# Kernel optimization log

Measured on AMD Instinct MI355X. Metric: run time of the kernel, lower is better.

Reference implementation:

```python
import jax, jax.numpy as jnp
import numpy as np

NEG_SLOPE = 0.2  # PyG GATConv default leaky_relu slope
EPS = 1e-16     # PyG softmax denominator epsilon


def gat_conv(x, src, dst, W, att_src, att_dst, bias, concat, num_nodes):
    """PyG-style GATConv (eval mode, dropout disabled).
    x: [N, F_in]; W: [F_in, H*C]; att_src/att_dst: [H, C]; bias: [H*C] or [C].
    Messages flow src -> dst; softmax is per destination node."""
    H, C = att_src.shape
    h = (x @ W).reshape(num_nodes, H, C)                      # [N,H,C]
    a_src = jnp.sum(h * att_src[None], axis=-1)               # [N,H]
    a_dst = jnp.sum(h * att_dst[None], axis=-1)               # [N,H]
    e = jax.nn.leaky_relu(a_src[src] + a_dst[dst], NEG_SLOPE) # [E,H]
    # numerically-stable segment softmax over edges grouped by dst
    m = jax.ops.segment_max(e, dst, num_segments=num_nodes)   # [N,H]
    ex = jnp.exp(e - m[dst])                                  # [E,H]
    s = jax.ops.segment_sum(ex, dst, num_segments=num_nodes)  # [N,H]
    alpha = ex / (s[dst] + EPS)                               # [E,H]
    msg = h[src] * alpha[..., None]                           # [E,H,C]
    out = jax.ops.segment_sum(msg, dst, num_segments=num_nodes)  # [N,H,C]
    if concat:
        out = out.reshape(num_nodes, H * C)
    else:
        out = out.mean(axis=1)                                # [N,C]
    return out + bias, alpha


def setup_inputs() -> dict:
    key = jax.random.key(0)
    ks = jax.random.split(key, 20)
    N, E = 50000, 500000
    F_node = 128       # num_node_features
    SED = 128          # sentence_embedding_dim
    HID = 64           # hidden_channels
    H = 2              # num_heads

    def g(k, shape, scale=0.05):
        return jax.random.normal(k, shape, dtype=jnp.float32) * scale

    return {
        "x": jax.random.normal(ks[0], (N, SED), dtype=jnp.float32),
        "edge_index": jax.random.randint(ks[1], (2, E), 0, N, dtype=jnp.int64),
        "cls_emb": jax.random.normal(ks[2], (768,), dtype=jnp.float32),
        # fc0: Linear(768, SED)
        "fc0_w": g(ks[3], (SED, 768)), "fc0_b": g(ks[4], (SED,)),
        # conv1: GATConv(2*SED -> HID, heads=H, concat=True)
        "W1": g(ks[5], (2 * SED, H * HID)),
        "att_src1": g(ks[6], (H, HID)), "att_dst1": g(ks[7], (H, HID)),
        "bias1": g(ks[8], (H * HID,)),
        # conv2: GATConv(H*HID -> F_node, heads=H, concat=False)
        "W2": g(ks[9], (H * HID, H * F_node)),
        "att_src2": g(ks[10], (H, F_node)), "att_dst2": g(ks[11], (H, F_node)),
        "bias2": g(ks[12], (F_node,)),
        # edge MLP head
        "fc2_w": g(ks[13], (F_node, 2 * F_node)), "fc2_b": g(ks[14], (F_node,)),
        "fc3_w": g(ks[15], (1, F_node)), "fc3_b": g(ks[16], (1,)),
    }


def reference(x, edge_index, cls_emb, fc0_w, fc0_b,
              W1, att_src1, att_dst1, bias1,
              W2, att_src2, att_dst2, bias2,
              fc2_w, fc2_b, fc3_w, fc3_b):
    N = x.shape[0]
    src, dst = edge_index[0], edge_index[1]
    # sentence embedding projection + broadcast-concat to every node
    sent = fc0_w @ cls_emb + fc0_b                                # [SED]
    h = jnp.concatenate([x, jnp.broadcast_to(sent, (N, sent.shape[0]))], axis=1)
    h, _ = gat_conv(h, src, dst, W1, att_src1, att_dst1, bias1, True, N)
    h = jax.nn.elu(h)
    h, _ = gat_conv(h, src, dst, W2, att_src2, att_dst2, bias2, False, N)
    # edge head: gather endpoints, concat, MLP, sigmoid
    edge_input = jnp.concatenate([h[src], h[dst]], axis=1)        # [E, 2*F]
    z = jax.nn.relu(edge_input @ fc2_w.T + fc2_b)                 # [E, F]
    logits = z @ fc3_w.T + fc3_b                                  # [E, 1]
    return jax.nn.sigmoid(logits)
```

## Files before the change

### kernel.cpp

```cpp
#include <hip/hip_runtime.h>
#include <hip/hip_bf16.h>
#include <math.h>


typedef short short8 __attribute__((ext_vector_type(8)));
typedef float floatx4 __attribute__((ext_vector_type(4)));
typedef float v2f __attribute__((ext_vector_type(2)));
typedef unsigned uint2v __attribute__((ext_vector_type(2)));

__device__ __forceinline__ v2f bfpair(unsigned v) {
    uint2v t; t.x = v << 16; t.y = v & 0xFFFF0000u;
    return __builtin_bit_cast(v2f, t);
}
__device__ __forceinline__ unsigned short bfbits(float f) {
    return __builtin_bit_cast(unsigned short, __float2bfloat16(f));
}
__device__ __forceinline__ unsigned packbf(float a, float b) {
    return ((unsigned)bfbits(b) << 16) | (unsigned)bfbits(a);
}
__device__ __forceinline__ float lrelu(float v) { return v > 0.f ? v : 0.2f * v; }

__global__ void prep_kernel(const float* __restrict__ cls, const float* __restrict__ fc0_w,
                            const float* __restrict__ fc0_b, const float* __restrict__ W1,
                            const float* __restrict__ W2, const float* __restrict__ fc2_w,
                            float* __restrict__ c1,
                            __hip_bfloat16* __restrict__ w1frag,
                            __hip_bfloat16* __restrict__ w2frag,
                            __hip_bfloat16* __restrict__ fc2frag) {
    int tid = threadIdx.x;
    if (blockIdx.x == 0) {
        __shared__ float s_sent[128];
        if (tid < 128) {
            float acc = fc0_b[tid];
            const float* row = fc0_w + (size_t)tid * 768;
            for (int k = 0; k < 768; ++k) acc += row[k] * cls[k];
            s_sent[tid] = acc;
        }
        __syncthreads();
        if (tid < 128) {
            float acc = 0.f;
            for (int k = 0; k < 128; ++k) acc += s_sent[k] * W1[(128 + k) * 128 + tid];
            c1[tid] = acc;
        }
    }
    int gstride = gridDim.x * blockDim.x;
    int g = blockIdx.x * blockDim.x + tid;
    for (int i = g; i < 16384; i += gstride) {
        int j = i & 7, l = (i >> 3) & 63, nt = (i >> 9) & 7, kt = (i >> 12) & 3;
        int k = kt * 32 + (l >> 4) * 8 + j;
        int n = nt * 16 + (l & 15);
        w1frag[i] = __float2bfloat16(W1[k * 128 + n]);
    }
    for (int i = g; i < 32768; i += gstride) {
        int j = i & 7, l = (i >> 3) & 63, nt = (i >> 9) & 15, kt = (i >> 13) & 3;
        int k = kt * 32 + (l >> 4) * 8 + j;
        int n = nt * 16 + (l & 15);
        w2frag[i] = __float2bfloat16(W2[k * 256 + n]);
    }
    for (int i = g; i < 32768; i += gstride) {
        int j = i & 7, l = (i >> 3) & 63, nt = (i >> 9) & 15, kt = (i >> 13) & 3;
        int k = kt * 32 + (l >> 4) * 8 + j;
        int n = nt * 16 + (l & 15);
        float v = (n < 128) ? fc2_w[n * 256 + k] : fc2_w[(n - 128) * 256 + 128 + k];
        fc2frag[i] = __float2bfloat16(v);
    }
}

__global__ void __launch_bounds__(256) bsum_kernel(const int* __restrict__ counts,
                                                   int* __restrict__ bsum, int N) {
    int base = blockIdx.x * 1024;
    int tid = threadIdx.x;
    int v = 0;
    #pragma unroll
    for (int k = 0; k < 4; ++k) {
        int idx = base + k * 256 + tid;
        if (idx < N) v += counts[idx];
    }
    #pragma unroll
    for (int off = 1; off < 64; off <<= 1) v += __shfl_xor(v, off, 64);
    __shared__ int ws[4];
    if ((tid & 63) == 0) ws[tid >> 6] = v;
    __syncthreads();
    if (tid == 0) bsum[blockIdx.x] = ws[0] + ws[1] + ws[2] + ws[3];
}

__global__ void top_scan_kernel(const int* __restrict__ bsum, int* __restrict__ boff, int nb) {
    int lane = threadIdx.x;
    int v = (lane < nb) ? bsum[lane] : 0;
    int x = v;
    #pragma unroll
    for (int off = 1; off < 64; off <<= 1) {
        int t = __shfl_up(x, off, 64);
        if (lane >= off) x += t;
    }
    if (lane < nb) boff[lane] = x - v;
}

__global__ void __launch_bounds__(1024) local_scan_kernel(const int* __restrict__ counts,
                                                          const int* __restrict__ boff,
                                                          int* __restrict__ row, int* __restrict__ woff,
                                                          int N, int E) {
    int tid = threadIdx.x, lane = tid & 63, wv = tid >> 6;
    int base = blockIdx.x * 1024;
    __shared__ int wsum[16];
    int v = (base + tid < N) ? counts[base + tid] : 0;
    int x = v;
    #pragma unroll
    for (int off = 1; off < 64; off <<= 1) {
        int t = __shfl_up(x, off, 64);
        if (lane >= off) x += t;
    }
    if (lane == 63) wsum[wv] = x;
    __syncthreads();
    if (wv == 0 && lane < 16) {
        int y = wsum[lane];
        #pragma unroll
        for (int off = 1; off < 16; off <<= 1) {
            int t = __shfl_up(y, off, 64);
            if (lane >= off) y += t;
        }
        wsum[lane] = y;
    }
    __syncthreads();
    int excl = boff[blockIdx.x] + (wv ? wsum[wv - 1] : 0) + x - v;
    if (base + tid < N) { row[base + tid] = excl; woff[base + tid] = excl; }
    if (blockIdx.x == 0 && tid == 0) row[N] = E;
}

__global__ void scatter_kernel(const int* __restrict__ src, const int* __restrict__ dst,
                               int* __restrict__ woff, int* __restrict__ srcs, int E) {
    int e = blockIdx.x * blockDim.x + threadIdx.x;
    if (e < E) {
        int pos = atomicAdd(&woff[dst[e]], 1);
        srcs[pos] = src[e];
    }
}

__global__ void __launch_bounds__(256) gemm1_count_kernel(
        const float* __restrict__ x, const __hip_bfloat16* __restrict__ wfrag,
        const float* __restrict__ c1, const float* __restrict__ att_s, const float* __restrict__ att_d,
        __hip_bfloat16* __restrict__ h1bf, float* __restrict__ a_src, float* __restrict__ a_dst,
        const int* __restrict__ dst, int* __restrict__ counts, int E, int G1, int N) {
    if ((int)blockIdx.x >= G1) {
        int e = ((int)blockIdx.x - G1) * 256 + threadIdx.x;
        if (e < E) atomicAdd(&counts[dst[e]], 1);
        return;
    }
    int lane = threadIdx.x & 63, wv = threadIdx.x >> 6;
    int lo = lane & 15, quad = lane >> 4;
    int rowbase = ((int)blockIdx.x * 4 + wv) * 16;
    if (rowbase >= N) return;
    int arow = rowbase + lo; if (arow >= N) arow = N - 1;
    const float* ap = x + (size_t)arow * 128 + quad * 8;
    floatx4 acc[8];
    #pragma unroll
    for (int nt = 0; nt < 8; ++nt) acc[nt] = (floatx4){0.f, 0.f, 0.f, 0.f};
    const short8* bf = (const short8*)wfrag;
    #pragma unroll
    for (int kt = 0; kt < 4; ++kt) {
        float4 fa = *(const float4*)(ap + kt * 32);
        float4 fb = *(const float4*)(ap + kt * 32 + 4);
        short8 a;
        a[0] = (short)bfbits(fa.x); a[1] = (short)bfbits(fa.y);
        a[2] = (short)bfbits(fa.z); a[3] = (short)bfbits(fa.w);
        a[4] = (short)bfbits(fb.x); a[5] = (short)bfbits(fb.y);
        a[6] = (short)bfbits(fb.z); a[7] = (short)bfbits(fb.w);
        #pragma unroll
        for (int nt = 0; nt < 8; ++nt)
            acc[nt] = __builtin_amdgcn_mfma_f32_16x16x32_bf16(a, bf[(kt * 8 + nt) * 64 + lane], acc[nt], 0, 0, 0);
    }
    float ps0[4] = {0,0,0,0}, ps1[4] = {0,0,0,0}, pd0[4] = {0,0,0,0}, pd1[4] = {0,0,0,0};
    #pragma unroll
    for (int nt = 0; nt < 8; ++nt) {
        int ch = nt * 16 + lo;
        float cv = c1[ch], as_v = att_s[ch], ad_v = att_d[ch];
        #pragma unroll
        for (int r = 0; r < 4; ++r) {
            int row = rowbase + quad * 4 + r;
            float val = acc[nt][r] + cv;
            if (row < N) ((unsigned short*)h1bf)[(size_t)row * 128 + ch] = bfbits(val);
            if (nt < 4) { ps0[r] += val * as_v; pd0[r] += val * ad_v; }
            else        { ps1[r] += val * as_v; pd1[r] += val * ad_v; }
        }
    }
    #pragma unroll
    for (int r = 0; r < 4; ++r) {
        int row = rowbase + quad * 4 + r;
        float v0 = ps0[r], v1 = ps1[r], v2 = pd0[r], v3 = pd1[r];
        #pragma unroll
        for (int off = 1; off < 16; off <<= 1) {
            v0 += __shfl_xor(v0, off, 64); v1 += __shfl_xor(v1, off, 64);
            v2 += __shfl_xor(v2, off, 64); v3 += __shfl_xor(v3, off, 64);
        }
        if (lo == 0 && row < N) {
            a_src[row * 2 + 0] = v0; a_src[row * 2 + 1] = v1;
            a_dst[row * 2 + 0] = v2; a_dst[row * 2 + 1] = v3;
        }
    }
}

__global__ void __launch_bounds__(256) agg1_csr_kernel(
        const int* __restrict__ row, const int* __restrict__ srcs,
        const float* __restrict__ a_src, const float* __restrict__ a_dst,
        const unsigned* __restrict__ h1u, const float* __restrict__ bias1,
        unsigned* __restrict__ hmid_u, int N) {
    int tid = threadIdx.x;
    int d = blockIdx.x * 16 + (tid >> 4);
    if (d >= N) return;
    int q = tid & 15;
    int beg = row[d], end = row[d + 1];
    float2 adp = ((const float2*)a_dst)[d];
    float den0 = 0.f, den1 = 0.f;
    v2f facc2[4];
    #pragma unroll
    for (int m = 0; m < 4; ++m) facc2[m] = (v2f){0.f, 0.f};
    for (int i = beg; i < end; i += 2) {
        int s0 = srcs[i];
        bool has1 = (i + 1) < end;
        int s1 = has1 ? srcs[i + 1] : s0;
        float2 as0 = ((const float2*)a_src)[s0];
        float2 as1 = ((const float2*)a_src)[s1];
        uint4 u0 = ((const uint4*)(h1u + (size_t)s0 * 64))[q];
        uint4 u1 = ((const uint4*)(h1u + (size_t)s1 * 64))[q];
        float e00 = __expf(lrelu(as0.x + adp.x));
        float e01 = __expf(lrelu(as0.y + adp.y));
        float e10 = has1 ? __expf(lrelu(as1.x + adp.x)) : 0.f;
        float e11 = has1 ? __expf(lrelu(as1.y + adp.y)) : 0.f;
        den0 += e00 + e10;
        den1 += e01 + e11;
        float w0 = (q < 8) ? e00 : e01;
        float w1 = (q < 8) ? e10 : e11;
        facc2[0] += bfpair(u0.x) * w0 + bfpair(u1.x) * w1;
        facc2[1] += bfpair(u0.y) * w0 + bfpair(u1.y) * w1;
        facc2[2] += bfpair(u0.z) * w0 + bfpair(u1.z) * w1;
        facc2[3] += bfpair(u0.w) * w0 + bfpair(u1.w) * w1;
    }
    float inv = 1.f / (((q < 8) ? den0 : den1) + 1e-16f);
    int c0 = 8 * q;
    float v[8];
    #pragma unroll
    for (int m = 0; m < 4; ++m) {
        float va = facc2[m].x * inv + bias1[c0 + 2 * m];
        float vb = facc2[m].y * inv + bias1[c0 + 2 * m + 1];
        v[2 * m]     = va > 0.f ? va : expm1f(va);
        v[2 * m + 1] = vb > 0.f ? vb : expm1f(vb);
    }
    uint4 o;
    o.x = packbf(v[0], v[1]); o.y = packbf(v[2], v[3]);
    o.z = packbf(v[4], v[5]); o.w = packbf(v[6], v[7]);
    ((uint4*)(hmid_u + (size_t)d * 64))[q] = o;
}

__global__ void __launch_bounds__(256) gemm2_mfma_kernel(
        const __hip_bfloat16* __restrict__ hmid, const __hip_bfloat16* __restrict__ wfrag,
        const float* __restrict__ att_s, const float* __restrict__ att_d,
        __hip_bfloat16* __restrict__ h2pre, float* __restrict__ a_src, float* __restrict__ a_dst, int N) {
    int lane = threadIdx.x & 63, wv = threadIdx.x >> 6;
    int lo = lane & 15, quad = lane >> 4;
    int rowbase = (blockIdx.x * 4 + wv) * 16;
    if (rowbase >= N) return;
    int arow = rowbase + lo; if (arow >= N) arow = N - 1;
    const __hip_bfloat16* ap = hmid + (size_t)arow * 128 + quad * 8;
    floatx4 acc[16];
    #pragma unroll
    for (int nt = 0; nt < 16; ++nt) acc[nt] = (floatx4){0.f, 0.f, 0.f, 0.f};
    const short8* bf = (const short8*)wfrag;
    #pragma unroll
    for (int kt = 0; kt < 4; ++kt) {
        short8 a = *(const short8*)(ap + kt * 32);
        #pragma unroll
        for (int nt = 0; nt < 16; ++nt)
            acc[nt] = __builtin_amdgcn_mfma_f32_16x16x32_bf16(a, bf[(kt * 16 + nt) * 64 + lane], acc[nt], 0, 0, 0);
    }
    float ps0[4] = {0,0,0,0}, ps1[4] = {0,0,0,0}, pd0[4] = {0,0,0,0}, pd1[4] = {0,0,0,0};
    #pragma unroll
    for (int nt = 0; nt < 16; ++nt) {
        int ch = nt * 16 + lo;
        float as_v = att_s[ch], ad_v = att_d[ch];
        #pragma unroll
        for (int r = 0; r < 4; ++r) {
            int row = rowbase + quad * 4 + r;
            float val = acc[nt][r];
            if (row < N) ((unsigned short*)h2pre)[(size_t)row * 256 + ch] = bfbits(val);
            if (nt < 8) { ps0[r] += val * as_v; pd0[r] += val * ad_v; }
            else        { ps1[r] += val * as_v; pd1[r] += val * ad_v; }
        }
    }
    #pragma unroll
    for (int r = 0; r < 4; ++r) {
        int row = rowbase + quad * 4 + r;
        float v0 = ps0[r], v1 = ps1[r], v2 = pd0[r], v3 = pd1[r];
        #pragma unroll
        for (int off = 1; off < 16; off <<= 1) {
            v0 += __shfl_xor(v0, off, 64); v1 += __shfl_xor(v1, off, 64);
            v2 += __shfl_xor(v2, off, 64); v3 += __shfl_xor(v3, off, 64);
        }
        if (lo == 0 && row < N) {
            a_src[row * 2 + 0] = v0; a_src[row * 2 + 1] = v1;
            a_dst[row * 2 + 0] = v2; a_dst[row * 2 + 1] = v3;
        }
    }
}

__global__ void __launch_bounds__(256) agg2_csr_kernel(
        const int* __restrict__ row, const int* __restrict__ srcs,
        const float* __restrict__ a_src, const float* __restrict__ a_dst,
        const unsigned* __restrict__ h2u, const float* __restrict__ bias2,
        unsigned* __restrict__ h2bf_u, int N) {
    int tid = threadIdx.x;
    int d = blockIdx.x * 8 + (tid >> 5);
    if (d >= N) return;
    int q = tid & 31;
    int beg = row[d], end = row[d + 1];
    float2 adp = ((const float2*)a_dst)[d];
    float den0 = 0.f, den1 = 0.f;
    v2f facc2[4];
    #pragma unroll
    for (int m = 0; m < 4; ++m) facc2[m] = (v2f){0.f, 0.f};
    for (int i = beg; i < end; i += 2) {
        int s0 = srcs[i];
        bool has1 = (i + 1) < end;
        int s1 = has1 ? srcs[i + 1] : s0;
        float2 as0 = ((const float2*)a_src)[s0];
        float2 as1 = ((const float2*)a_src)[s1];
        uint4 u0 = ((const uint4*)(h2u + (size_t)s0 * 128))[q];
        uint4 u1 = ((const uint4*)(h2u + (size_t)s1 * 128))[q];
        float e00 = __expf(lrelu(as0.x + adp.x));
        float e01 = __expf(lrelu(as0.y + adp.y));
        float e10 = has1 ? __expf(lrelu(as1.x + adp.x)) : 0.f;
        float e11 = has1 ? __expf(lrelu(as1.y + adp.y)) : 0.f;
        den0 += e00 + e10;
        den1 += e01 + e11;
        float w0 = (q < 16) ? e00 : e01;
        float w1 = (q < 16) ? e10 : e11;
        facc2[0] += bfpair(u0.x) * w0 + bfpair(u1.x) * w1;
        facc2[1] += bfpair(u0.y) * w0 + bfpair(u1.y) * w1;
        facc2[2] += bfpair(u0.z) * w0 + bfpair(u1.z) * w1;
        facc2[3] += bfpair(u0.w) * w0 + bfpair(u1.w) * w1;
    }
    float inv = 0.5f / (((q < 16) ? den0 : den1) + 1e-16f);
    #pragma unroll
    for (int m = 0; m < 4; ++m) {
        facc2[m] *= inv;
        facc2[m].x += __shfl_xor(facc2[m].x, 16, 64);
        facc2[m].y += __shfl_xor(facc2[m].y, 16, 64);
    }
    if (q < 16) {
        int c0 = 8 * q;
        uint4 o;
        o.x = packbf(facc2[0].x + bias2[c0 + 0], facc2[0].y + bias2[c0 + 1]);
        o.y = packbf(facc2[1].x + bias2[c0 + 2], facc2[1].y + bias2[c0 + 3]);
        o.z = packbf(facc2[2].x + bias2[c0 + 4], facc2[2].y + bias2[c0 + 5]);
        o.w = packbf(facc2[3].x + bias2[c0 + 6], facc2[3].y + bias2[c0 + 7]);
        ((uint4*)(h2bf_u + (size_t)d * 64))[q] = o;
    }
}

__global__ void __launch_bounds__(256) zsd_mfma_kernel(
        const __hip_bfloat16* __restrict__ h2bf, const __hip_bfloat16* __restrict__ wfrag,
        const float* __restrict__ fc2_b, __hip_bfloat16* __restrict__ zsd, int N) {
    int lane = threadIdx.x & 63, wv = threadIdx.x >> 6;
    int lo = lane & 15, quad = lane >> 4;
    int rowbase = (blockIdx.x * 4 + wv) * 16;
    if (rowbase >= N) return;
    int arow = rowbase + lo; if (arow >= N) arow = N - 1;
    const __hip_bfloat16* ap = h2bf + (size_t)arow * 128 + quad * 8;
    floatx4 acc[16];
    #pragma unroll
    for (int nt = 0; nt < 16; ++nt) acc[nt] = (floatx4){0.f, 0.f, 0.f, 0.f};
    const short8* bf = (const short8*)wfrag;
    #pragma unroll
    for (int kt = 0; kt < 4; ++kt) {
        short8 a = *(const short8*)(ap + kt * 32);
        #pragma unroll
        for (int nt = 0; nt < 16; ++nt)
            acc[nt] = __builtin_amdgcn_mfma_f32_16x16x32_bf16(a, bf[(kt * 16 + nt) * 64 + lane], acc[nt], 0, 0, 0);
    }
    #pragma unroll
    for (int nt = 0; nt < 16; ++nt) {
        int ch = nt * 16 + lo;
        float bv = (nt >= 8) ? fc2_b[ch - 128] : 0.f;
        #pragma unroll
        for (int r = 0; r < 4; ++r) {
            int row = rowbase + quad * 4 + r;
            if (row < N) ((unsigned short*)zsd)[(size_t)row * 256 + ch] = bfbits(acc[nt][r] + bv);
        }
    }
}

__global__ void __launch_bounds__(256) edge_zsd_kernel(
        const int* __restrict__ src, const int* __restrict__ dst,
        const unsigned* __restrict__ zsd_u, const float* __restrict__ fc3_w,
        const float* __restrict__ fc3_b, float* __restrict__ out, int E) {
    int lane = threadIdx.x & 63, wv = threadIdx.x >> 6;
    int g = lane >> 5, r = (lane >> 4) & 1, q = lane & 15;
    int base = (blockIdx.x * 4 + wv) * 16;
    if (base >= E) return;
    v2f f30 = {fc3_w[8 * q + 4 * r + 0], fc3_w[8 * q + 4 * r + 1]};
    v2f f31 = {fc3_w[8 * q + 4 * r + 2], fc3_w[8 * q + 4 * r + 3]};
    float b3 = fc3_b[0];
    int nodes[8];
    #pragma unroll
    for (int j = 0; j < 8; ++j) {
        int e = base + 2 * j + g;
        int ec = e < E ? e : E - 1;
        nodes[j] = r ? dst[ec] : src[ec];
    }
    uint4 rows[8];
    #pragma unroll
    for (int j = 0; j < 8; ++j)
        rows[j] = ((const uint4*)(zsd_u + (size_t)nodes[j] * 128 + (r << 6)))[q];
    #pragma unroll
    for (int j = 0; j < 8; ++j) {
        uint4 mine = rows[j];
        unsigned sx = (unsigned)__shfl_xor((int)mine.x, 16, 64);
        unsigned sy = (unsigned)__shfl_xor((int)mine.y, 16, 64);
        unsigned sz = (unsigned)__shfl_xor((int)mine.z, 16, 64);
        unsigned sw = (unsigned)__shfl_xor((int)mine.w, 16, 64);
        unsigned mA = r ? mine.z : mine.x;
        unsigned mB = r ? mine.w : mine.y;
        unsigned oA = r ? sz : sx;
        unsigned oB = r ? sw : sy;
        v2f sA = bfpair(mA) + bfpair(oA);
        v2f sB = bfpair(mB) + bfpair(oB);
        sA.x = fmaxf(sA.x, 0.f); sA.y = fmaxf(sA.y, 0.f);
        sB.x = fmaxf(sB.x, 0.f); sB.y = fmaxf(sB.y, 0.f);
        v2f p2 = sA * f30 + sB * f31;
        float p = p2.x + p2.y;
        #pragma unroll
        for (int off = 1; off < 32; off <<= 1) p += __shfl_xor(p, off, 64);
        int e = base + 2 * j + g;
        if ((lane & 31) == 0 && e < E)
            out[e] = 1.f / (1.f + expf(-(p + b3)));
    }
}

extern "C" void kernel_launch(void* const* d_in, const int* in_sizes, int n_in,
                              void* d_out, int out_size, void* d_ws, size_t ws_size,
                              hipStream_t stream) {
    const float* x      = (const float*)d_in[0];
    const int*   ei     = (const int*)d_in[1];
    const float* cls    = (const float*)d_in[2];
    const float* fc0_w  = (const float*)d_in[3];
    const float* fc0_b  = (const float*)d_in[4];
    const float* W1     = (const float*)d_in[5];
    const float* att_s1 = (const float*)d_in[6];
    const float* att_d1 = (const float*)d_in[7];
    const float* bias1  = (const float*)d_in[8];
    const float* W2     = (const float*)d_in[9];
    const float* att_s2 = (const float*)d_in[10];
    const float* att_d2 = (const float*)d_in[11];
    const float* bias2  = (const float*)d_in[12];
    const float* fc2_w  = (const float*)d_in[13];
    const float* fc2_b  = (const float*)d_in[14];
    const float* fc3_w  = (const float*)d_in[15];
    const float* fc3_b  = (const float*)d_in[16];
    float* out = (float*)d_out;

    int N = in_sizes[0] / 128;
    int E = in_sizes[1] / 2;
    const int* src = ei;
    const int* dst = ei + E;
    int nb = (N + 1023) / 1024;

    float* w = (float*)d_ws;
    size_t off = 0;
    auto alloc = [&](size_t n) { float* p = w + off; off += (n + 63) & ~(size_t)63; return p; };
    float* c1      = alloc(128);
    float* w1fragf = alloc(16384 / 2);
    float* w2fragf = alloc(32768 / 2);
    float* fc2fragf= alloc(32768 / 2);
    float* a_s1    = alloc((size_t)N * 2);
    float* a_d1    = alloc((size_t)N * 2);
    float* a_s2    = alloc((size_t)N * 2);
    float* a_d2    = alloc((size_t)N * 2);
    float* h1bff   = alloc((size_t)N * 64);
    float* hmidf   = alloc((size_t)N * 64);
    float* h2pref  = alloc((size_t)N * 128);
    float* h2bff   = alloc((size_t)N * 64);
    float* zsdf    = alloc((size_t)N * 128);
    int* counts = (int*)alloc(N);
    int* rowp   = (int*)alloc(N + 1);
    int* woff   = (int*)alloc(N);
    int* srcs   = (int*)alloc(E);
    int* bsum   = (int*)alloc(64);
    int* boff   = (int*)alloc(64);
    __hip_bfloat16* w1frag = (__hip_bfloat16*)w1fragf;
    __hip_bfloat16* w2frag = (__hip_bfloat16*)w2fragf;
    __hip_bfloat16* fc2frag= (__hip_bfloat16*)fc2fragf;
    __hip_bfloat16* hmid   = (__hip_bfloat16*)hmidf;
    __hip_bfloat16* h2pre  = (__hip_bfloat16*)h2pref;
    __hip_bfloat16* h2bf   = (__hip_bfloat16*)h2bff;
    __hip_bfloat16* h1bf   = (__hip_bfloat16*)h1bff;
    __hip_bfloat16* zsd    = (__hip_bfloat16*)zsdf;

    hipMemsetAsync(counts, 0, sizeof(int) * (size_t)N, stream);

    prep_kernel<<<64, 256, 0, stream>>>(cls, fc0_w, fc0_b, W1, W2, fc2_w, c1, w1frag, w2frag, fc2frag);
    int G1 = (N + 63) / 64;
    int G2 = (E + 255) / 256;
    gemm1_count_kernel<<<G1 + G2, 256, 0, stream>>>(x, w1frag, c1, att_s1, att_d1, h1bf, a_s1, a_d1,
                                                    dst, counts, E, G1, N);
    bsum_kernel<<<nb, 256, 0, stream>>>(counts, bsum, N);
    top_scan_kernel<<<1, 64, 0, stream>>>(bsum, boff, nb);
    local_scan_kernel<<<nb, 1024, 0, stream>>>(counts, boff, rowp, woff, N, E);
    scatter_kernel<<<(E + 255) / 256, 256, 0, stream>>>(src, dst, woff, srcs, E);
    agg1_csr_kernel<<<(N + 15) / 16, 256, 0, stream>>>(rowp, srcs, a_s1, a_d1, (const unsigned*)h1bf, bias1, (unsigned*)hmid, N);
    gemm2_mfma_kernel<<<(N + 63) / 64, 256, 0, stream>>>(hmid, w2frag, att_s2, att_d2, h2pre, a_s2, a_d2, N);
    agg2_csr_kernel<<<(N + 7) / 8, 256, 0, stream>>>(rowp, srcs, a_s2, a_d2, (const unsigned*)h2pre, bias2, (unsigned*)h2bf, N);
    zsd_mfma_kernel<<<(N + 63) / 64, 256, 0, stream>>>(h2bf, fc2frag, fc2_b, zsd, N);
    edge_zsd_kernel<<<(E + 63) / 64, 256, 0, stream>>>(src, dst, (const unsigned*)zsd, fc3_w, fc3_b, out, E);
}
```

Baseline: 336.3 us.

## Fuse all stages into one cooperative persistent kernel with grid syncs

Replaces the sequence of about eleven kernel launches and a memset with a single cooperative mega-kernel that loops over tiles persistently and uses grid.sync between stages. The aim is to remove per-launch overhead and the gaps between dependent kernels. In exchange, every stage shares one register and occupancy budget capped by the heaviest stage (launch_bounds 256,4). It also adds grid-wide barrier costs and host occupancy queries on each call, and the local scan is restructured to four elements per thread.

```diff
diff --git a/kernel.cpp b/kernel.cpp
--- a/kernel.cpp
+++ b/kernel.cpp
@@ -1,6 +1,9 @@
 #include <hip/hip_runtime.h>
+#include <hip/hip_cooperative_groups.h>
 #include <hip/hip_bf16.h>
 #include <math.h>
+
+namespace cg = cooperative_groups;
 
 
 typedef short short8 __attribute__((ext_vector_type(8)));
@@ -20,448 +23,441 @@
 }
 __device__ __forceinline__ float lrelu(float v) { return v > 0.f ? v : 0.2f * v; }
 
-__global__ void prep_kernel(const float* __restrict__ cls, const float* __restrict__ fc0_w,
-                            const float* __restrict__ fc0_b, const float* __restrict__ W1,
-                            const float* __restrict__ W2, const float* __restrict__ fc2_w,
-                            float* __restrict__ c1,
-                            __hip_bfloat16* __restrict__ w1frag,
-                            __hip_bfloat16* __restrict__ w2frag,
-                            __hip_bfloat16* __restrict__ fc2frag) {
-    int tid = threadIdx.x;
+struct MegaParams {
+    const float* x; const int* src; const int* dst;
+    const float* cls; const float* fc0_w; const float* fc0_b;
+    const float* W1; const float* att_s1; const float* att_d1; const float* bias1;
+    const float* W2; const float* att_s2; const float* att_d2; const float* bias2;
+    const float* fc2_w; const float* fc2_b; const float* fc3_w; const float* fc3_b;
+    float* out;
+    float* c1; __hip_bfloat16* w1frag; __hip_bfloat16* w2frag; __hip_bfloat16* fc2frag;
+    float* a_s1; float* a_d1; float* a_s2; float* a_d2;
+    __hip_bfloat16* h1bf; __hip_bfloat16* hmid; __hip_bfloat16* h2pre;
+    __hip_bfloat16* h2bf; __hip_bfloat16* zsd;
+    int* counts; int* rowp; int* woff; int* srcs; int* bsum; int* boff;
+    int N, E, nb;
+};
+
+__global__ void __launch_bounds__(256, 4) mega_kernel(MegaParams p) {
+    cg::grid_group grid = cg::this_grid();
+    const int tid = threadIdx.x;
+    const int G = gridDim.x;
+    const int lane = tid & 63, wv = tid >> 6;
+    const int lo = lane & 15, quad = lane >> 4;
+    const int N = p.N, E = p.E;
+
+    __shared__ float s_sent[128];
+    __shared__ int s_wsum[16];
+
+    for (int i = blockIdx.x * 256 + tid; i < N; i += G * 256) p.counts[i] = 0;
     if (blockIdx.x == 0) {
-        __shared__ float s_sent[128];
         if (tid < 128) {
-            float acc = fc0_b[tid];
-            const float* row = fc0_w + (size_t)tid * 768;
-            for (int k = 0; k < 768; ++k) acc += row[k] * cls[k];
+            float acc = p.fc0_b[tid];
+            const float* row = p.fc0_w + (size_t)tid * 768;
+            for (int k = 0; k < 768; ++k) acc += row[k] * p.cls[k];
             s_sent[tid] = acc;
         }
         __syncthreads();
         if (tid < 128) {
             float acc = 0.f;
-            for (int k = 0; k < 128; ++k) acc += s_sent[k] * W1[(128 + k) * 128 + tid];
-            c1[tid] = acc;
-        }
-    }
-    int gstride = gridDim.x * blockDim.x;
-    int g = blockIdx.x * blockDim.x + tid;
-    for (int i = g; i < 16384; i += gstride) {
-        int j = i & 7, l = (i >> 3) & 63, nt = (i >> 9) & 7, kt = (i >> 12) & 3;
-        int k = kt * 32 + (l >> 4) * 8 + j;
-        int n = nt * 16 + (l & 15);
-        w1frag[i] = __float2bfloat16(W1[k * 128 + n]);
-    }
-    for (int i = g; i < 32768; i += gstride) {
-        int j = i & 7, l = (i >> 3) & 63, nt = (i >> 9) & 15, kt = (i >> 13) & 3;
-        int k = kt * 32 + (l >> 4) * 8 + j;
-        int n = nt * 16 + (l & 15);
-        w2frag[i] = __float2bfloat16(W2[k * 256 + n]);
-    }
-    for (int i = g; i < 32768; i += gstride) {
-        int j = i & 7, l = (i >> 3) & 63, nt = (i >> 9) & 15, kt = (i >> 13) & 3;
-        int k = kt * 32 + (l >> 4) * 8 + j;
-        int n = nt * 16 + (l & 15);
-        float v = (n < 128) ? fc2_w[n * 256 + k] : fc2_w[(n - 128) * 256 + 128 + k];
-        fc2frag[i] = __float2bfloat16(v);
-    }
-}
-
-__global__ void __launch_bounds__(256) bsum_kernel(const int* __restrict__ counts,
-                                                   int* __restrict__ bsum, int N) {
-    int base = blockIdx.x * 1024;
-    int tid = threadIdx.x;
-    int v = 0;
-    #pragma unroll
-    for (int k = 0; k < 4; ++k) {
-        int idx = base + k * 256 + tid;
-        if (idx < N) v += counts[idx];
-    }
-    #pragma unroll
-    for (int off = 1; off < 64; off <<= 1) v += __shfl_xor(v, off, 64);
-    __shared__ int ws[4];
-    if ((tid & 63) == 0) ws[tid >> 6] = v;
-    __syncthreads();
-    if (tid == 0) bsum[blockIdx.x] = ws[0] + ws[1] + ws[2] + ws[3];
-}
-
-__global__ void top_scan_kernel(const int* __restrict__ bsum, int* __restrict__ boff, int nb) {
-    int lane = threadIdx.x;
-    int v = (lane < nb) ? bsum[lane] : 0;
-    int x = v;
-    #pragma unroll
-    for (int off = 1; off < 64; off <<= 1) {
-        int t = __shfl_up(x, off, 64);
-        if (lane >= off) x += t;
-    }
-    if (lane < nb) boff[lane] = x - v;
-}
-
-__global__ void __launch_bounds__(1024) local_scan_kernel(const int* __restrict__ counts,
-                                                          const int* __restrict__ boff,
-                                                          int* __restrict__ row, int* __restrict__ woff,
-                                                          int N, int E) {
-    int tid = threadIdx.x, lane = tid & 63, wv = tid >> 6;
-    int base = blockIdx.x * 1024;
-    __shared__ int wsum[16];
-    int v = (base + tid < N) ? counts[base + tid] : 0;
-    int x = v;
-    #pragma unroll
-    for (int off = 1; off < 64; off <<= 1) {
-        int t = __shfl_up(x, off, 64);
-        if (lane >= off) x += t;
-    }
-    if (lane == 63) wsum[wv] = x;
-    __syncthreads();
-    if (wv == 0 && lane < 16) {
-        int y = wsum[lane];
+            for (int k = 0; k < 128; ++k) acc += s_sent[k] * p.W1[(128 + k) * 128 + tid];
+            p.c1[tid] = acc;
+        }
+    }
+    {
+        int g = blockIdx.x * 256 + tid, gs = G * 256;
+        for (int i = g; i < 16384; i += gs) {
+            int j = i & 7, l = (i >> 3) & 63, nt = (i >> 9) & 7, kt = (i >> 12) & 3;
+            int k = kt * 32 + (l >> 4) * 8 + j;
+            int n = nt * 16 + (l & 15);
+            p.w1frag[i] = __float2bfloat16(p.W1[k * 128 + n]);
+        }
+        for (int i = g; i < 32768; i += gs) {
+            int j = i & 7, l = (i >> 3) & 63, nt = (i >> 9) & 15, kt = (i >> 13) & 3;
+            int k = kt * 32 + (l >> 4) * 8 + j;
+            int n = nt * 16 + (l & 15);
+            p.w2frag[i] = __float2bfloat16(p.W2[k * 256 + n]);
+        }
+        for (int i = g; i < 32768; i += gs) {
+            int j = i & 7, l = (i >> 3) & 63, nt = (i >> 9) & 15, kt = (i >> 13) & 3;
+            int k = kt * 32 + (l >> 4) * 8 + j;
+            int n = nt * 16 + (l & 15);
+            float v = (n < 128) ? p.fc2_w[n * 256 + k] : p.fc2_w[(n - 128) * 256 + 128 + k];
+            p.fc2frag[i] = __float2bfloat16(v);
+        }
+    }
+    grid.sync();
+
+    {
+        int T = (N + 63) / 64;
+        const short8* bf = (const short8*)p.w1frag;
+        for (int tb = blockIdx.x; tb < T; tb += G) {
+            int rowbase = (tb * 4 + wv) * 16;
+            if (rowbase < N) {
+                int arow = rowbase + lo; if (arow >= N) arow = N - 1;
+                const float* ap = p.x + (size_t)arow * 128 + quad * 8;
+                floatx4 acc[8];
+                #pragma unroll
+                for (int nt = 0; nt < 8; ++nt) acc[nt] = (floatx4){0.f, 0.f, 0.f, 0.f};
+                #pragma unroll
+                for (int kt = 0; kt < 4; ++kt) {
+                    float4 fa = *(const float4*)(ap + kt * 32);
+                    float4 fb = *(const float4*)(ap + kt * 32 + 4);
+                    short8 a;
+                    a[0] = (short)bfbits(fa.x); a[1] = (short)bfbits(fa.y);
+                    a[2] = (short)bfbits(fa.z); a[3] = (short)bfbits(fa.w);
+                    a[4] = (short)bfbits(fb.x); a[5] = (short)bfbits(fb.y);
+                    a[6] = (short)bfbits(fb.z); a[7] = (short)bfbits(fb.w);
+                    #pragma unroll
+                    for (int nt = 0; nt < 8; ++nt)
+                        acc[nt] = __builtin_amdgcn_mfma_f32_16x16x32_bf16(a, bf[(kt * 8 + nt) * 64 + lane], acc[nt], 0, 0, 0);
+                }
+                float ps0[4] = {0,0,0,0}, ps1[4] = {0,0,0,0}, pd0[4] = {0,0,0,0}, pd1[4] = {0,0,0,0};
+                #pragma unroll
+                for (int nt = 0; nt < 8; ++nt) {
+                    int ch = nt * 16 + lo;
+                    float cv = p.c1[ch], as_v = p.att_s1[ch], ad_v = p.att_d1[ch];
+                    #pragma unroll
+                    for (int r = 0; r < 4; ++r) {
+                        int row = rowbase + quad * 4 + r;
+                        float val = acc[nt][r] + cv;
+                        if (row < N) ((unsigned short*)p.h1bf)[(size_t)row * 128 + ch] = bfbits(val);
+                        if (nt < 4) { ps0[r] += val * as_v; pd0[r] += val * ad_v; }
+                        else        { ps1[r] += val * as_v; pd1[r] += val * ad_v; }
+                    }
+                }
+                #pragma unroll
+                for (int r = 0; r < 4; ++r) {
+                    int row = rowbase + quad * 4 + r;
+                    float v0 = ps0[r], v1 = ps1[r], v2 = pd0[r], v3 = pd1[r];
+                    #pragma unroll
+                    for (int off = 1; off < 16; off <<= 1) {
+                        v0 += __shfl_xor(v0, off, 64); v1 += __shfl_xor(v1, off, 64);
+                        v2 += __shfl_xor(v2, off, 64); v3 += __shfl_xor(v3, off, 64);
+                    }
+                    if (lo == 0 && row < N) {
+                        p.a_s1[row * 2 + 0] = v0; p.a_s1[row * 2 + 1] = v1;
+                        p.a_d1[row * 2 + 0] = v2; p.a_d1[row * 2 + 1] = v3;
+                    }
+                }
+            }
+        }
+        for (int e = blockIdx.x * 256 + tid; e < E; e += G * 256)
+            atomicAdd(&p.counts[p.dst[e]], 1);
+    }
+    grid.sync();
+
+    for (int tb = blockIdx.x; tb < p.nb; tb += G) {
+        int base = tb * 1024;
+        int v = 0;
         #pragma unroll
-        for (int off = 1; off < 16; off <<= 1) {
-            int t = __shfl_up(y, off, 64);
-            if (lane >= off) y += t;
-        }
-        wsum[lane] = y;
-    }
-    __syncthreads();
-    int excl = boff[blockIdx.x] + (wv ? wsum[wv - 1] : 0) + x - v;
-    if (base + tid < N) { row[base + tid] = excl; woff[base + tid] = excl; }
-    if (blockIdx.x == 0 && tid == 0) row[N] = E;
-}
-
-__global__ void scatter_kernel(const int* __restrict__ src, const int* __restrict__ dst,
-                               int* __restrict__ woff, int* __restrict__ srcs, int E) {
-    int e = blockIdx.x * blockDim.x + threadIdx.x;
-    if (e < E) {
-        int pos = atomicAdd(&woff[dst[e]], 1);
-        srcs[pos] = src[e];
-    }
-}
-
-__global__ void __launch_bounds__(256) gemm1_count_kernel(
-        const float* __restrict__ x, const __hip_bfloat16* __restrict__ wfrag,
-        const float* __restrict__ c1, const float* __restrict__ att_s, const float* __restrict__ att_d,
-        __hip_bfloat16* __restrict__ h1bf, float* __restrict__ a_src, float* __restrict__ a_dst,
-        const int* __restrict__ dst, int* __restrict__ counts, int E, int G1, int N) {
-    if ((int)blockIdx.x >= G1) {
-        int e = ((int)blockIdx.x - G1) * 256 + threadIdx.x;
-        if (e < E) atomicAdd(&counts[dst[e]], 1);
-        return;
-    }
-    int lane = threadIdx.x & 63, wv = threadIdx.x >> 6;
-    int lo = lane & 15, quad = lane >> 4;
-    int rowbase = ((int)blockIdx.x * 4 + wv) * 16;
-    if (rowbase >= N) return;
-    int arow = rowbase + lo; if (arow >= N) arow = N - 1;
-    const float* ap = x + (size_t)arow * 128 + quad * 8;
-    floatx4 acc[8];
-    #pragma unroll
-    for (int nt = 0; nt < 8; ++nt) acc[nt] = (floatx4){0.f, 0.f, 0.f, 0.f};
-    const short8* bf = (const short8*)wfrag;
-    #pragma unroll
-    for (int kt = 0; kt < 4; ++kt) {
-        float4 fa = *(const float4*)(ap + kt * 32);
-        float4 fb = *(const float4*)(ap + kt * 32 + 4);
-        short8 a;
-        a[0] = (short)bfbits(fa.x); a[1] = (short)bfbits(fa.y);
-        a[2] = (short)bfbits(fa.z); a[3] = (short)bfbits(fa.w);
-        a[4] = (short)bfbits(fb.x); a[5] = (short)bfbits(fb.y);
-        a[6] = (short)bfbits(fb.z); a[7] = (short)bfbits(fb.w);
+        for (int k = 0; k < 4; ++k) {
+            int idx = base + k * 256 + tid;
+            if (idx < N) v += p.counts[idx];
+        }
         #pragma unroll
-        for (int nt = 0; nt < 8; ++nt)
-            acc[nt] = __builtin_amdgcn_mfma_f32_16x16x32_bf16(a, bf[(kt * 8 + nt) * 64 + lane], acc[nt], 0, 0, 0);
-    }
-    float ps0[4] = {0,0,0,0}, ps1[4] = {0,0,0,0}, pd0[4] = {0,0,0,0}, pd1[4] = {0,0,0,0};
-    #pragma unroll
-    for (int nt = 0; nt < 8; ++nt) {
-        int ch = nt * 16 + lo;
-        float cv = c1[ch], as_v = att_s[ch], ad_v = att_d[ch];
+        for (int off = 1; off < 64; off <<= 1) v += __shfl_xor(v, off, 64);
+        if (lane == 0) s_wsum[wv] = v;
+        __syncthreads();
+        if (tid == 0) p.bsum[tb] = s_wsum[0] + s_wsum[1] + s_wsum[2] + s_wsum[3];
+        __syncthreads();
+    }
+    grid.sync();
+
+    if (blockIdx.x == 0 && tid < 64) {
+        int v = (tid < p.nb) ? p.bsum[tid] : 0;
+        int x = v;
         #pragma unroll
-        for (int r = 0; r < 4; ++r) {
-            int row = rowbase + quad * 4 + r;
-            float val = acc[nt][r] + cv;
-            if (row < N) ((unsigned short*)h1bf)[(size_t)row * 128 + ch] = bfbits(val);
-            if (nt < 4) { ps0[r] += val * as_v; pd0[r] += val * ad_v; }
-            else        { ps1[r] += val * as_v; pd1[r] += val * ad_v; }
-        }
-    }
-    #pragma unroll
-    for (int r = 0; r < 4; ++r) {
-        int row = rowbase + quad * 4 + r;
-        float v0 = ps0[r], v1 = ps1[r], v2 = pd0[r], v3 = pd1[r];
+        for (int off = 1; off < 64; off <<= 1) {
+            int t = __shfl_up(x, off, 64);
+            if (tid >= off) x += t;
+        }
+        if (tid < p.nb) p.boff[tid] = x - v;
+    }
+    grid.sync();
+
+    for (int tb = blockIdx.x; tb < p.nb; tb += G) {
+        int i0 = tb * 1024 + tid * 4;
+        int c[4]; int tsum = 0;
         #pragma unroll
-        for (int off = 1; off < 16; off <<= 1) {
-            v0 += __shfl_xor(v0, off, 64); v1 += __shfl_xor(v1, off, 64);
-            v2 += __shfl_xor(v2, off, 64); v3 += __shfl_xor(v3, off, 64);
-        }
-        if (lo == 0 && row < N) {
-            a_src[row * 2 + 0] = v0; a_src[row * 2 + 1] = v1;
-            a_dst[row * 2 + 0] = v2; a_dst[row * 2 + 1] = v3;
-        }
-    }
-}
-
-__global__ void __launch_bounds__(256) agg1_csr_kernel(
-        const int* __restrict__ row, const int* __restrict__ srcs,
-        const float* __restrict__ a_src, const float* __restrict__ a_dst,
-        const unsigned* __restrict__ h1u, const float* __restrict__ bias1,
-        unsigned* __restrict__ hmid_u, int N) {
-    int tid = threadIdx.x;
-    int d = blockIdx.x * 16 + (tid >> 4);
-    if (d >= N) return;
-    int q = tid & 15;
-    int beg = row[d], end = row[d + 1];
-    float2 adp = ((const float2*)a_dst)[d];
-    float den0 = 0.f, den1 = 0.f;
-    v2f facc2[4];
-    #pragma unroll
-    for (int m = 0; m < 4; ++m) facc2[m] = (v2f){0.f, 0.f};
-    for (int i = beg; i < end; i += 2) {
-        int s0 = srcs[i];
-        bool has1 = (i + 1) < end;
-        int s1 = has1 ? srcs[i + 1] : s0;
-        float2 as0 = ((const float2*)a_src)[s0];
-        float2 as1 = ((const float2*)a_src)[s1];
-        uint4 u0 = ((const uint4*)(h1u + (size_t)s0 * 64))[q];
-        uint4 u1 = ((const uint4*)(h1u + (size_t)s1 * 64))[q];
-        float e00 = __expf(lrelu(as0.x + adp.x));
-        float e01 = __expf(lrelu(as0.y + adp.y));
-        float e10 = has1 ? __expf(lrelu(as1.x + adp.x)) : 0.f;
-        float e11 = has1 ? __expf(lrelu(as1.y + adp.y)) : 0.f;
-        den0 += e00 + e10;
-        den1 += e01 + e11;
-        float w0 = (q < 8) ? e00 : e01;
-        float w1 = (q < 8) ? e10 : e11;
-        facc2[0] += bfpair(u0.x) * w0 + bfpair(u1.x) * w1;
-        facc2[1] += bfpair(u0.y) * w0 + bfpair(u1.y) * w1;
-        facc2[2] += bfpair(u0.z) * w0 + bfpair(u1.z) * w1;
-        facc2[3] += bfpair(u0.w) * w0 + bfpair(u1.w) * w1;
-    }
-    float inv = 1.f / (((q < 8) ? den0 : den1) + 1e-16f);
-    int c0 = 8 * q;
-    float v[8];
-    #pragma unroll
-    for (int m = 0; m < 4; ++m) {
-        float va = facc2[m].x * inv + bias1[c0 + 2 * m];
-        float vb = facc2[m].y * inv + bias1[c0 + 2 * m + 1];
-        v[2 * m]     = va > 0.f ? va : expm1f(va);
-        v[2 * m + 1] = vb > 0.f ? vb : expm1f(vb);
-    }
-    uint4 o;
-    o.x = packbf(v[0], v[1]); o.y = packbf(v[2], v[3]);
-    o.z = packbf(v[4], v[5]); o.w = packbf(v[6], v[7]);
-    ((uint4*)(hmid_u + (size_t)d * 64))[q] = o;
-}
-
-__global__ void __launch_bounds__(256) gemm2_mfma_kernel(
-        const __hip_bfloat16* __restrict__ hmid, const __hip_bfloat16* __restrict__ wfrag,
-        const float* __restrict__ att_s, const float* __restrict__ att_d,
-        __hip_bfloat16* __restrict__ h2pre, float* __restrict__ a_src, float* __restrict__ a_dst, int N) {
-    int lane = threadIdx.x & 63, wv = threadIdx.x >> 6;
-    int lo = lane & 15, quad = lane >> 4;
-    int rowbase = (blockIdx.x * 4 + wv) * 16;
-    if (rowbase >= N) return;
-    int arow = rowbase + lo; if (arow >= N) arow = N - 1;
-    const __hip_bfloat16* ap = hmid + (size_t)arow * 128 + quad * 8;
-    floatx4 acc[16];
-    #pragma unroll
-    for (int nt = 0; nt < 16; ++nt) acc[nt] = (floatx4){0.f, 0.f, 0.f, 0.f};
-    const short8* bf = (const short8*)wfrag;
-    #pragma unroll
-    for (int kt = 0; kt < 4; ++kt) {
-        short8 a = *(const short8*)(ap + kt * 32);
+        for (int k = 0; k < 4; ++k) {
+            c[k] = (i0 + k < N) ? p.counts[i0 + k] : 0;
+            tsum += c[k];
+        }
+        int x = tsum;
         #pragma unroll
-        for (int nt = 0; nt < 16; ++nt)
-            acc[nt] = __builtin_amdgcn_mfma_f32_16x16x32_bf16(a, bf[(kt * 16 + nt) * 64 + lane], acc[nt], 0, 0, 0);
-    }
-    float ps0[4] = {0,0,0,0}, ps1[4] = {0,0,0,0}, pd0[4] = {0,0,0,0}, pd1[4] = {0,0,0,0};
-    #pragma unroll
-    for (int nt = 0; nt < 16; ++nt) {
-        int ch = nt * 16 + lo;
-        float as_v = att_s[ch], ad_v = att_d[ch];
+        for (int off = 1; off < 64; off <<= 1) {
+            int t = __shfl_up(x, off, 64);
+            if (lane >= off) x += t;
+        }
+        if (lane == 63) s_wsum[wv] = x;
+        __syncthreads();
+        int add = 0;
+        for (int w = 0; w < wv; ++w) add += s_wsum[w];
+        int run = p.boff[tb] + add + x - tsum;
         #pragma unroll
-        for (int r = 0; r < 4; ++r) {
-            int row = rowbase + quad * 4 + r;
-            float val = acc[nt][r];
-            if (row < N) ((unsigned short*)h2pre)[(size_t)row * 256 + ch] = bfbits(val);
-            if (nt < 8) { ps0[r] += val * as_v; pd0[r] += val * ad_v; }
-            else        { ps1[r] += val * as_v; pd1[r] += val * ad_v; }
-        }
-    }
-    #pragma unroll
-    for (int r = 0; r < 4; ++r) {
-        int row = rowbase + quad * 4 + r;
-        float v0 = ps0[r], v1 = ps1[r], v2 = pd0[r], v3 = pd1[r];
-        #pragma unroll
-        for (int off = 1; off < 16; off <<= 1) {
-            v0 += __shfl_xor(v0, off, 64); v1 += __shfl_xor(v1, off, 64);
-            v2 += __shfl_xor(v2, off, 64); v3 += __shfl_xor(v3, off, 64);
-        }
-        if (lo == 0 && row < N) {
-            a_src[row * 2 + 0] = v0; a_src[row * 2 + 1] = v1;
-            a_dst[row * 2 + 0] = v2; a_dst[row * 2 + 1] = v3;
-        }
-    }
-}
-
-__global__ void __launch_bounds__(256) agg2_csr_kernel(
-        const int* __restrict__ row, const int* __restrict__ srcs,
-        const float* __restrict__ a_src, const float* __restrict__ a_dst,
-        const unsigned* __restrict__ h2u, const float* __restrict__ bias2,
-        unsigned* __restrict__ h2bf_u, int N) {
-    int tid = threadIdx.x;
-    int d = blockIdx.x * 8 + (tid >> 5);
-    if (d >= N) return;
-    int q = tid & 31;
-    int beg = row[d], end = row[d + 1];
-    float2 adp = ((const float2*)a_dst)[d];
-    float den0 = 0.f, den1 = 0.f;
-    v2f facc2[4];
-    #pragma unroll
-    for (int m = 0; m < 4; ++m) facc2[m] = (v2f){0.f, 0.f};
-    for (int i = beg; i < end; i += 2) {
-        int s0 = srcs[i];
-        bool has1 = (i + 1) < end;
-        int s1 = has1 ? srcs[i + 1] : s0;
-        float2 as0 = ((const float2*)a_src)[s0];
-        float2 as1 = ((const float2*)a_src)[s1];
-        uint4 u0 = ((const uint4*)(h2u + (size_t)s0 * 128))[q];
-        uint4 u1 = ((const uint4*)(h2u + (size_t)s1 * 128))[q];
-        float e00 = __expf(lrelu(as0.x + adp.x));
-        float e01 = __expf(lrelu(as0.y + adp.y));
-        float e10 = has1 ? __expf(lrelu(as1.x + adp.x)) : 0.f;
-        float e11 = has1 ? __expf(lrelu(as1.y + adp.y)) : 0.f;
-        den0 += e00 + e10;
-        den1 += e01 + e11;
-        float w0 = (q < 16) ? e00 : e01;
-        float w1 = (q < 16) ? e10 : e11;
-        facc2[0] += bfpair(u0.x) * w0 + bfpair(u1.x) * w1;
-        facc2[1] += bfpair(u0.y) * w0 + bfpair(u1.y) * w1;
-        facc2[2] += bfpair(u0.z) * w0 + bfpair(u1.z) * w1;
-        facc2[3] += bfpair(u0.w) * w0 + bfpair(u1.w) * w1;
-    }
-    float inv = 0.5f / (((q < 16) ? den0 : den1) + 1e-16f);
-    #pragma unroll
-    for (int m = 0; m < 4; ++m) {
-        facc2[m] *= inv;
-        facc2[m].x += __shfl_xor(facc2[m].x, 16, 64);
-        facc2[m].y += __shfl_xor(facc2[m].y, 16, 64);
-    }
-    if (q < 16) {
-        int c0 = 8 * q;
-        uint4 o;
-        o.x = packbf(facc2[0].x + bias2[c0 + 0], facc2[0].y + bias2[c0 + 1]);
-        o.y = packbf(facc2[1].x + bias2[c0 + 2], facc2[1].y + bias2[c0 + 3]);
-        o.z = packbf(facc2[2].x + bias2[c0 + 4], facc2[2].y + bias2[c0 + 5]);
-        o.w = packbf(facc2[3].x + bias2[c0 + 6], facc2[3].y + bias2[c0 + 7]);
-        ((uint4*)(h2bf_u + (size_t)d * 64))[q] = o;
-    }
-}
-
-__global__ void __launch_bounds__(256) zsd_mfma_kernel(
-        const __hip_bfloat16* __restrict__ h2bf, const __hip_bfloat16* __restrict__ wfrag,
-        const float* __restrict__ fc2_b, __hip_bfloat16* __restrict__ zsd, int N) {
-    int lane = threadIdx.x & 63, wv = threadIdx.x >> 6;
-    int lo = lane & 15, quad = lane >> 4;
-    int rowbase = (blockIdx.x * 4 + wv) * 16;
-    if (rowbase >= N) return;
-    int arow = rowbase + lo; if (arow >= N) arow = N - 1;
-    const __hip_bfloat16* ap = h2bf + (size_t)arow * 128 + quad * 8;
-    floatx4 acc[16];
-    #pragma unroll
-    for (int nt = 0; nt < 16; ++nt) acc[nt] = (floatx4){0.f, 0.f, 0.f, 0.f};
-    const short8* bf = (const short8*)wfrag;
-    #pragma unroll
-    for (int kt = 0; kt < 4; ++kt) {
-        short8 a = *(const short8*)(ap + kt * 32);
-        #pragma unroll
-        for (int nt = 0; nt < 16; ++nt)
-            acc[nt] = __builtin_amdgcn_mfma_f32_16x16x32_bf16(a, bf[(kt * 16 + nt) * 64 + lane], acc[nt], 0, 0, 0);
-    }
-    #pragma unroll
-    for (int nt = 0; nt < 16; ++nt) {
-        int ch = nt * 16 + lo;
-        float bv = (nt >= 8) ? fc2_b[ch - 128] : 0.f;
-        #pragma unroll
-        for (int r = 0; r < 4; ++r) {
-            int row = rowbase + quad * 4 + r;
-            if (row < N) ((unsigned short*)zsd)[(size_t)row * 256 + ch] = bfbits(acc[nt][r] + bv);
-        }
-    }
-}
-
-__global__ void __launch_bounds__(256) edge_zsd_kernel(
-        const int* __restrict__ src, const int* __restrict__ dst,
-        const unsigned* __restrict__ zsd_u, const float* __restrict__ fc3_w,
-        const float* __restrict__ fc3_b, float* __restrict__ out, int E) {
-    int lane = threadIdx.x & 63, wv = threadIdx.x >> 6;
-    int g = lane >> 5, r = (lane >> 4) & 1, q = lane & 15;
-    int base = (blockIdx.x * 4 + wv) * 16;
-    if (base >= E) return;
-    v2f f30 = {fc3_w[8 * q + 4 * r + 0], fc3_w[8 * q + 4 * r + 1]};
-    v2f f31 = {fc3_w[8 * q + 4 * r + 2], fc3_w[8 * q + 4 * r + 3]};
-    float b3 = fc3_b[0];
-    int nodes[8];
-    #pragma unroll
-    for (int j = 0; j < 8; ++j) {
-        int e = base + 2 * j + g;
-        int ec = e < E ? e : E - 1;
-        nodes[j] = r ? dst[ec] : src[ec];
-    }
-    uint4 rows[8];
-    #pragma unroll
-    for (int j = 0; j < 8; ++j)
-        rows[j] = ((const uint4*)(zsd_u + (size_t)nodes[j] * 128 + (r << 6)))[q];
-    #pragma unroll
-    for (int j = 0; j < 8; ++j) {
-        uint4 mine = rows[j];
-        unsigned sx = (unsigned)__shfl_xor((int)mine.x, 16, 64);
-        unsigned sy = (unsigned)__shfl_xor((int)mine.y, 16, 64);
-        unsigned sz = (unsigned)__shfl_xor((int)mine.z, 16, 64);
-        unsigned sw = (unsigned)__shfl_xor((int)mine.w, 16, 64);
-        unsigned mA = r ? mine.z : mine.x;
-        unsigned mB = r ? mine.w : mine.y;
-        unsigned oA = r ? sz : sx;
-        unsigned oB = r ? sw : sy;
-        v2f sA = bfpair(mA) + bfpair(oA);
-        v2f sB = bfpair(mB) + bfpair(oB);
-        sA.x = fmaxf(sA.x, 0.f); sA.y = fmaxf(sA.y, 0.f);
-        sB.x = fmaxf(sB.x, 0.f); sB.y = fmaxf(sB.y, 0.f);
-        v2f p2 = sA * f30 + sB * f31;
-        float p = p2.x + p2.y;
-        #pragma unroll
-        for (int off = 1; off < 32; off <<= 1) p += __shfl_xor(p, off, 64);
-        int e = base + 2 * j + g;
-        if ((lane & 31) == 0 && e < E)
-            out[e] = 1.f / (1.f + expf(-(p + b3)));
+        for (int k = 0; k < 4; ++k) {
+            if (i0 + k < N) { p.rowp[i0 + k] = run; p.woff[i0 + k] = run; }
+            run += c[k];
+        }
+        __syncthreads();
+    }
+    if (blockIdx.x == 0 && tid == 0) p.rowp[N] = E;
+    grid.sync();
+
+    for (int e = blockIdx.x * 256 + tid; e < E; e += G * 256) {
+        int pos = atomicAdd(&p.woff[p.dst[e]], 1);
+        p.srcs[pos] = p.src[e];
+    }
+    grid.sync();
+
+    {
+        int T = (N + 15) / 16;
+        const unsigned* h1u = (const unsigned*)p.h1bf;
+        for (int tb = blockIdx.x; tb < T; tb += G) {
+            int d = tb * 16 + (tid >> 4);
+            if (d < N) {
+                int q = tid & 15;
+                int beg = p.rowp[d], end = p.rowp[d + 1];
+                float2 adp = ((const float2*)p.a_d1)[d];
+                float den0 = 0.f, den1 = 0.f;
+                v2f facc2[4];
+                #pragma unroll
+                for (int m = 0; m < 4; ++m) facc2[m] = (v2f){0.f, 0.f};
+                for (int i = beg; i < end; i += 2) {
+                    int s0 = p.srcs[i];
+                    bool has1 = (i + 1) < end;
+                    int s1 = has1 ? p.srcs[i + 1] : s0;
+                    float2 as0 = ((const float2*)p.a_s1)[s0];
+                    float2 as1 = ((const float2*)p.a_s1)[s1];
+                    uint4 u0 = ((const uint4*)(h1u + (size_t)s0 * 64))[q];
+                    uint4 u1 = ((const uint4*)(h1u + (size_t)s1 * 64))[q];
+                    float e00 = __expf(lrelu(as0.x + adp.x));
+                    float e01 = __expf(lrelu(as0.y + adp.y));
+                    float e10 = has1 ? __expf(lrelu(as1.x + adp.x)) : 0.f;
+                    float e11 = has1 ? __expf(lrelu(as1.y + adp.y)) : 0.f;
+                    den0 += e00 + e10;
+                    den1 += e01 + e11;
+                    float w0 = (q < 8) ? e00 : e01;
+                    float w1 = (q < 8) ? e10 : e11;
+                    facc2[0] += bfpair(u0.x) * w0 + bfpair(u1.x) * w1;
+                    facc2[1] += bfpair(u0.y) * w0 + bfpair(u1.y) * w1;
+                    facc2[2] += bfpair(u0.z) * w0 + bfpair(u1.z) * w1;
+                    facc2[3] += bfpair(u0.w) * w0 + bfpair(u1.w) * w1;
+                }
+                float inv = 1.f / (((q < 8) ? den0 : den1) + 1e-16f);
+                int c0 = 8 * q;
+                float v[8];
+                #pragma unroll
+                for (int m = 0; m < 4; ++m) {
+                    float va = facc2[m].x * inv + p.bias1[c0 + 2 * m];
+                    float vb = facc2[m].y * inv + p.bias1[c0 + 2 * m + 1];
+                    v[2 * m]     = va > 0.f ? va : expm1f(va);
+                    v[2 * m + 1] = vb > 0.f ? vb : expm1f(vb);
+                }
+                uint4 o;
+                o.x = packbf(v[0], v[1]); o.y = packbf(v[2], v[3]);
+                o.z = packbf(v[4], v[5]); o.w = packbf(v[6], v[7]);
+                ((uint4*)((unsigned*)p.hmid + (size_t)d * 64))[q] = o;
+            }
+        }
+    }
+    grid.sync();
+
+    {
+        int T = (N + 63) / 64;
+        const short8* bf = (const short8*)p.w2frag;
+        for (int tb = blockIdx.x; tb < T; tb += G) {
+            int rowbase = (tb * 4 + wv) * 16;
+            if (rowbase < N) {
+                int arow = rowbase + lo; if (arow >= N) arow = N - 1;
+                const __hip_bfloat16* ap = p.hmid + (size_t)arow * 128 + quad * 8;
+                floatx4 acc[16];
+                #pragma unroll
+                for (int nt = 0; nt < 16; ++nt) acc[nt] = (floatx4){0.f, 0.f, 0.f, 0.f};
+                #pragma unroll
+                for (int kt = 0; kt < 4; ++kt) {
+                    short8 a = *(const short8*)(ap + kt * 32);
+                    #pragma unroll
+                    for (int nt = 0; nt < 16; ++nt)
+                        acc[nt] = __builtin_amdgcn_mfma_f32_16x16x32_bf16(a, bf[(kt * 16 + nt) * 64 + lane], acc[nt], 0, 0, 0);
+                }
+                float ps0[4] = {0,0,0,0}, ps1[4] = {0,0,0,0}, pd0[4] = {0,0,0,0}, pd1[4] = {0,0,0,0};
+                #pragma unroll
+                for (int nt = 0; nt < 16; ++nt) {
+                    int ch = nt * 16 + lo;
+                    float as_v = p.att_s2[ch], ad_v = p.att_d2[ch];
+                    #pragma unroll
+                    for (int r = 0; r < 4; ++r) {
+                        int row = rowbase + quad * 4 + r;
+                        float val = acc[nt][r];
+                        if (row < N) ((unsigned short*)p.h2pre)[(size_t)row * 256 + ch] = bfbits(val);
+                        if (nt < 8) { ps0[r] += val * as_v; pd0[r] += val * ad_v; }
+                        else        { ps1[r] += val * as_v; pd1[r] += val * ad_v; }
+                    }
+                }
+                #pragma unroll
+                for (int r = 0; r < 4; ++r) {
+                    int row = rowbase + quad * 4 + r;
+                    float v0 = ps0[r], v1 = ps1[r], v2 = pd0[r], v3 = pd1[r];
+                    #pragma unroll
+                    for (int off = 1; off < 16; off <<= 1) {
+                        v0 += __shfl_xor(v0, off, 64); v1 += __shfl_xor(v1, off, 64);
+                        v2 += __shfl_xor(v2, off, 64); v3 += __shfl_xor(v3, off, 64);
+                    }
+                    if (lo == 0 && row < N) {
+                        p.a_s2[row * 2 + 0] = v0; p.a_s2[row * 2 + 1] = v1;
+                        p.a_d2[row * 2 + 0] = v2; p.a_d2[row * 2 + 1] = v3;
+                    }
+                }
+            }
+        }
+    }
+    grid.sync();
+
+    {
+        int T = (N + 7) / 8;
+        const unsigned* h2u = (const unsigned*)p.h2pre;
+        for (int tb = blockIdx.x; tb < T; tb += G) {
+            int d = tb * 8 + (tid >> 5);
+            if (d < N) {
+                int q = tid & 31;
+                int beg = p.rowp[d], end = p.rowp[d + 1];
+                float2 adp = ((const float2*)p.a_d2)[d];
+                float den0 = 0.f, den1 = 0.f;
+                v2f facc2[4];
+                #pragma unroll
+                for (int m = 0; m < 4; ++m) facc2[m] = (v2f){0.f, 0.f};
+                for (int i = beg; i < end; i += 2) {
+                    int s0 = p.srcs[i];
+                    bool has1 = (i + 1) < end;
+                    int s1 = has1 ? p.srcs[i + 1] : s0;
+                    float2 as0 = ((const float2*)p.a_s2)[s0];
+                    float2 as1 = ((const float2*)p.a_s2)[s1];
+                    uint4 u0 = ((const uint4*)(h2u + (size_t)s0 * 128))[q];
+                    uint4 u1 = ((const uint4*)(h2u + (size_t)s1 * 128))[q];
+                    float e00 = __expf(lrelu(as0.x + adp.x));
+                    float e01 = __expf(lrelu(as0.y + adp.y));
+                    float e10 = has1 ? __expf(lrelu(as1.x + adp.x)) : 0.f;
+                    float e11 = has1 ? __expf(lrelu(as1.y + adp.y)) : 0.f;
+                    den0 += e00 + e10;
+                    den1 += e01 + e11;
+                    float w0 = (q < 16) ? e00 : e01;
+                    float w1 = (q < 16) ? e10 : e11;
+                    facc2[0] += bfpair(u0.x) * w0 + bfpair(u1.x) * w1;
+                    facc2[1] += bfpair(u0.y) * w0 + bfpair(u1.y) * w1;
+                    facc2[2] += bfpair(u0.z) * w0 + bfpair(u1.z) * w1;
+                    facc2[3] += bfpair(u0.w) * w0 + bfpair(u1.w) * w1;
+                }
+                float inv = 0.5f / (((q < 16) ? den0 : den1) + 1e-16f);
+                #pragma unroll
+                for (int m = 0; m < 4; ++m) {
+                    facc2[m] *= inv;
+                    facc2[m].x += __shfl_xor(facc2[m].x, 16, 64);
+                    facc2[m].y += __shfl_xor(facc2[m].y, 16, 64);
+                }
+                if (q < 16) {
+                    int c0 = 8 * q;
+                    uint4 o;
+                    o.x = packbf(facc2[0].x + p.bias2[c0 + 0], facc2[0].y + p.bias2[c0 + 1]);
+                    o.y = packbf(facc2[1].x + p.bias2[c0 + 2], facc2[1].y + p.bias2[c0 + 3]);
+                    o.z = packbf(facc2[2].x + p.bias2[c0 + 4], facc2[2].y + p.bias2[c0 + 5]);
+                    o.w = packbf(facc2[3].x + p.bias2[c0 + 6], facc2[3].y + p.bias2[c0 + 7]);
+                    ((uint4*)((unsigned*)p.h2bf + (size_t)d * 64))[q] = o;
+                }
+            }
+        }
+    }
+    grid.sync();
+
+    {
+        int T = (N + 63) / 64;
+        const short8* bf = (const short8*)p.fc2frag;
+        for (int tb = blockIdx.x; tb < T; tb += G) {
+            int rowbase = (tb * 4 + wv) * 16;
+            if (rowbase < N) {
+                int arow = rowbase + lo; if (arow >= N) arow = N - 1;
+                const __hip_bfloat16* ap = p.h2bf + (size_t)arow * 128 + quad * 8;
+                floatx4 acc[16];
+                #pragma unroll
+                for (int nt = 0; nt < 16; ++nt) acc[nt] = (floatx4){0.f, 0.f, 0.f, 0.f};
+                #pragma unroll
+                for (int kt = 0; kt < 4; ++kt) {
+                    short8 a = *(const short8*)(ap + kt * 32);
+                    #pragma unroll
+                    for (int nt = 0; nt < 16; ++nt)
+                        acc[nt] = __builtin_amdgcn_mfma_f32_16x16x32_bf16(a, bf[(kt * 16 + nt) * 64 + lane], acc[nt], 0, 0, 0);
+                }
+                #pragma unroll
+                for (int nt = 0; nt < 16; ++nt) {
+                    int ch = nt * 16 + lo;
+                    float bv = (nt >= 8) ? p.fc2_b[ch - 128] : 0.f;
+                    #pragma unroll
+                    for (int r = 0; r < 4; ++r) {
+                        int row = rowbase + quad * 4 + r;
+                        if (row < N) ((unsigned short*)p.zsd)[(size_t)row * 256 + ch] = bfbits(acc[nt][r] + bv);
+                    }
+                }
+            }
+        }
+    }
+    grid.sync();
+
+    {
+        int T = (E + 63) / 64;
+        const unsigned* zsd_u = (const unsigned*)p.zsd;
+        int g = lane >> 5, r = (lane >> 4) & 1, q = lane & 15;
+        v2f f30 = {p.fc3_w[8 * q + 4 * r + 0], p.fc3_w[8 * q + 4 * r + 1]};
+        v2f f31 = {p.fc3_w[8 * q + 4 * r + 2], p.fc3_w[8 * q + 4 * r + 3]};
+        float b3 = p.fc3_b[0];
+        for (int tb = blockIdx.x; tb < T; tb += G) {
+            int base = (tb * 4 + wv) * 16;
+            if (base < E) {
+                int nodes[8];
+                #pragma unroll
+                for (int j = 0; j < 8; ++j) {
+                    int e = base + 2 * j + g;
+                    int ec = e < E ? e : E - 1;
+                    nodes[j] = r ? p.dst[ec] : p.src[ec];
+                }
+                uint4 rows[8];
+                #pragma unroll
+                for (int j = 0; j < 8; ++j)
+                    rows[j] = ((const uint4*)(zsd_u + (size_t)nodes[j] * 128 + (r << 6)))[q];
+                #pragma unroll
+                for (int j = 0; j < 8; ++j) {
+                    uint4 mine = rows[j];
+                    unsigned sx = (unsigned)__shfl_xor((int)mine.x, 16, 64);
+                    unsigned sy = (unsigned)__shfl_xor((int)mine.y, 16, 64);
+                    unsigned sz = (unsigned)__shfl_xor((int)mine.z, 16, 64);
+                    unsigned sw = (unsigned)__shfl_xor((int)mine.w, 16, 64);
+                    unsigned mA = r ? mine.z : mine.x;
+                    unsigned mB = r ? mine.w : mine.y;
+                    unsigned oA = r ? sz : sx;
+                    unsigned oB = r ? sw : sy;
+                    v2f sA = bfpair(mA) + bfpair(oA);
+                    v2f sB = bfpair(mB) + bfpair(oB);
+                    sA.x = fmaxf(sA.x, 0.f); sA.y = fmaxf(sA.y, 0.f);
+                    sB.x = fmaxf(sB.x, 0.f); sB.y = fmaxf(sB.y, 0.f);
+                    v2f p2 = sA * f30 + sB * f31;
+                    float pp = p2.x + p2.y;
+                    #pragma unroll
+                    for (int off = 1; off < 32; off <<= 1) pp += __shfl_xor(pp, off, 64);
+                    int e = base + 2 * j + g;
+                    if ((lane & 31) == 0 && e < E)
+                        p.out[e] = 1.f / (1.f + expf(-(pp + b3)));
+                }
+            }
+        }
     }
 }
 
 extern "C" void kernel_launch(void* const* d_in, const int* in_sizes, int n_in,
                               void* d_out, int out_size, void* d_ws, size_t ws_size,
                               hipStream_t stream) {
-    const float* x      = (const float*)d_in[0];
-    const int*   ei     = (const int*)d_in[1];
-    const float* cls    = (const float*)d_in[2];
-    const float* fc0_w  = (const float*)d_in[3];
-    const float* fc0_b  = (const float*)d_in[4];
-    const float* W1     = (const float*)d_in[5];
-    const float* att_s1 = (const float*)d_in[6];
-    const float* att_d1 = (const float*)d_in[7];
-    const float* bias1  = (const float*)d_in[8];
-    const float* W2     = (const float*)d_in[9];
-    const float* att_s2 = (const float*)d_in[10];
-    const float* att_d2 = (const float*)d_in[11];
-    const float* bias2  = (const float*)d_in[12];
-    const float* fc2_w  = (const float*)d_in[13];
-    const float* fc2_b  = (const float*)d_in[14];
-    const float* fc3_w  = (const float*)d_in[15];
-    const float* fc3_b  = (const float*)d_in[16];
-    float* out = (float*)d_out;
-
     int N = in_sizes[0] / 128;
     int E = in_sizes[1] / 2;
-    const int* src = ei;
-    const int* dst = ei + E;
-    int nb = (N + 1023) / 1024;
+    const int* ei = (const int*)d_in[1];
 
     float* w = (float*)d_ws;
     size_t off = 0;
@@ -485,29 +481,41 @@
     int* srcs   = (int*)alloc(E);
     int* bsum   = (int*)alloc(64);
     int* boff   = (int*)alloc(64);
-    __hip_bfloat16* w1frag = (__hip_bfloat16*)w1fragf;
-    __hip_bfloat16* w2frag = (__hip_bfloat16*)w2fragf;
-    __hip_bfloat16* fc2frag= (__hip_bfloat16*)fc2fragf;
-    __hip_bfloat16* hmid   = (__hip_bfloat16*)hmidf;
-    __hip_bfloat16* h2pre  = (__hip_bfloat16*)h2pref;
-    __hip_bfloat16* h2bf   = (__hip_bfloat16*)h2bff;
-    __hip_bfloat16* h1bf   = (__hip_bfloat16*)h1bff;
-    __hip_bfloat16* zsd    = (__hip_bfloat16*)zsdf;
-
-    hipMemsetAsync(counts, 0, sizeof(int) * (size_t)N, stream);
-
-    prep_kernel<<<64, 256, 0, stream>>>(cls, fc0_w, fc0_b, W1, W2, fc2_w, c1, w1frag, w2frag, fc2frag);
-    int G1 = (N + 63) / 64;
-    int G2 = (E + 255) / 256;
-    gemm1_count_kernel<<<G1 + G2, 256, 0, stream>>>(x, w1frag, c1, att_s1, att_d1, h1bf, a_s1, a_d1,
-                                                    dst, counts, E, G1, N);
-    bsum_kernel<<<nb, 256, 0, stream>>>(counts, bsum, N);
-    top_scan_kernel<<<1, 64, 0, stream>>>(bsum, boff, nb);
-    local_scan_kernel<<<nb, 1024, 0, stream>>>(counts, boff, rowp, woff, N, E);
-    scatter_kernel<<<(E + 255) / 256, 256, 0, stream>>>(src, dst, woff, srcs, E);
-    agg1_csr_kernel<<<(N + 15) / 16, 256, 0, stream>>>(rowp, srcs, a_s1, a_d1, (const unsigned*)h1bf, bias1, (unsigned*)hmid, N);
-    gemm2_mfma_kernel<<<(N + 63) / 64, 256, 0, stream>>>(hmid, w2frag, att_s2, att_d2, h2pre, a_s2, a_d2, N);
-    agg2_csr_kernel<<<(N + 7) / 8, 256, 0, stream>>>(rowp, srcs, a_s2, a_d2, (const unsigned*)h2pre, bias2, (unsigned*)h2bf, N);
-    zsd_mfma_kernel<<<(N + 63) / 64, 256, 0, stream>>>(h2bf, fc2frag, fc2_b, zsd, N);
-    edge_zsd_kernel<<<(E + 63) / 64, 256, 0, stream>>>(src, dst, (const unsigned*)zsd, fc3_w, fc3_b, out, E);
+
+    MegaParams p;
+    p.x = (const float*)d_in[0];
+    p.src = ei; p.dst = ei + E;
+    p.cls = (const float*)d_in[2]; p.fc0_w = (const float*)d_in[3]; p.fc0_b = (const float*)d_in[4];
+    p.W1 = (const float*)d_in[5]; p.att_s1 = (const float*)d_in[6]; p.att_d1 = (const float*)d_in[7];
+    p.bias1 = (const float*)d_in[8];
+    p.W2 = (const float*)d_in[9]; p.att_s2 = (const float*)d_in[10]; p.att_d2 = (const float*)d_in[11];
+    p.bias2 = (const float*)d_in[12];
+    p.fc2_w = (const float*)d_in[13]; p.fc2_b = (const float*)d_in[14];
+    p.fc3_w = (const float*)d_in[15]; p.fc3_b = (const float*)d_in[16];
+    p.out = (float*)d_out;
+    p.c1 = c1;
+    p.w1frag = (__hip_bfloat16*)w1fragf;
+    p.w2frag = (__hip_bfloat16*)w2fragf;
+    p.fc2frag = (__hip_bfloat16*)fc2fragf;
+    p.a_s1 = a_s1; p.a_d1 = a_d1; p.a_s2 = a_s2; p.a_d2 = a_d2;
+    p.h1bf = (__hip_bfloat16*)h1bff;
+    p.hmid = (__hip_bfloat16*)hmidf;
+    p.h2pre = (__hip_bfloat16*)h2pref;
+    p.h2bf = (__hip_bfloat16*)h2bff;
+    p.zsd = (__hip_bfloat16*)zsdf;
+    p.counts = counts; p.rowp = rowp; p.woff = woff; p.srcs = srcs;
+    p.bsum = bsum; p.boff = boff;
+    p.N = N; p.E = E; p.nb = (N + 1023) / 1024;
+
+    int blocksPerCU = 0;
+    hipOccupancyMaxActiveBlocksPerMultiprocessor(&blocksPerCU, mega_kernel, 256, 0);
+    int numCU = 0;
+    hipDeviceGetAttribute(&numCU, hipDeviceAttributeMultiprocessorCount, 0);
+    if (blocksPerCU < 1) blocksPerCU = 1;
+    if (numCU < 1) numCU = 256;
+    int grid = blocksPerCU * numCU;
+    if (grid > 1024) grid = 1024;
+
+    void* args[] = {&p};
+    hipLaunchCooperativeKernel((void*)mega_kernel, dim3(grid), dim3(256), args, 0, stream);
 }
```

Result: slower. 1.101 ms (+227.4%).
